# Performance work log

Measured on AMD Instinct MI355X. Metric: run time of the kernel, lower is better.

Reference implementation:

```python
import jax, jax.numpy as jnp
import numpy as np

N_NODES = 50000
N_EDGES = 1600000
N_FEAT = 128
DROPOUT = 0.1


def setup_inputs() -> dict:
    key = jax.random.key(0)
    k1, k2, k3, k4 = jax.random.split(key, 4)
    x = jax.random.normal(k1, (N_NODES, N_FEAT), dtype=jnp.float32)
    adj_vals = jax.random.uniform(k2, (N_EDGES,), dtype=jnp.float32)
    row = jax.random.randint(k3, (N_EDGES,), 0, N_NODES, dtype=jnp.int32)
    col = jax.random.randint(k4, (N_EDGES,), 0, N_NODES, dtype=jnp.int32)
    return {"x": x, "adj_vals": adj_vals, "row": row, "col": col}


def reference(x, adj_vals, row, col):
    # MixedDropout on sparse adjacency values (deterministic fixed key),
    # then SpMM: out[i] = sum_{e: row[e]==i} A_drop[e] * x[col[e]]
    keep_prob = 1.0 - DROPOUT
    mask_key = jax.random.fold_in(jax.random.key(42), 7)
    keep = jax.random.bernoulli(mask_key, keep_prob, adj_vals.shape)
    vals_drop = jnp.where(keep, adj_vals / keep_prob, 0.0)
    # gather source features and weight by (dropped) edge values
    msgs = vals_drop[:, None] * x[col]  # [E, F]
    out = jax.ops.segment_sum(msgs, row, num_segments=N_NODES)  # [N, F]
    return out
```

## Files before the change

### kernel.cpp

```cpp
#include <hip/hip_runtime.h>
#include <stdint.h>

#define N_NODES 50000
#define N_EDGES 1600000
#define N_FEAT 128
#define CAP 64
#define OVF_CAP 65536

#define NB 98
#define RSHIFT 9
#define NWG_A 256
#define CAPW 88
#define EPW (N_EDGES / NWG_A)


struct KeyPair { uint32_t a, b; };

__host__ __device__ constexpr inline uint32_t rotl32(uint32_t x, int r) {
  return (x << r) | (x >> (32 - r));
}

__host__ __device__ constexpr inline KeyPair threefry2x32(uint32_t k0, uint32_t k1,
                                                          uint32_t x0, uint32_t x1) {
  const uint32_t ks0 = k0, ks1 = k1, ks2 = k0 ^ k1 ^ 0x1BD11BDAu;
  x0 += ks0;
  x1 += ks1;
  const int rotA[4] = {13, 15, 26, 6};
  const int rotB[4] = {17, 29, 16, 24};
  const uint32_t ks[3] = {ks0, ks1, ks2};
  for (int i = 0; i < 5; ++i) {
    const int* rot = (i & 1) ? rotB : rotA;
    for (int j = 0; j < 4; ++j) {
      x0 += x1;
      x1 = rotl32(x1, rot[j]);
      x1 ^= x0;
    }
    x0 += ks[(i + 1) % 3];
    x1 += ks[(i + 2) % 3] + (uint32_t)(i + 1);
  }
  return {x0, x1};
}

constexpr KeyPair MASK_KEY = threefry2x32(0u, 42u, 0u, 7u);

__device__ inline bool edge_keep(uint32_t e) {
  KeyPair r = threefry2x32(MASK_KEY.a, MASK_KEY.b, 0u, e);
  uint32_t bits = r.a ^ r.b;
  float u = __uint_as_float((bits >> 9) | 0x3f800000u) - 1.0f;
  return u < 0.9f;
}

__device__ inline uint32_t f2bf(uint32_t b) {
  return (b + 0x7fffu + ((b >> 16) & 1u)) >> 16;
}


__global__ void __launch_bounds__(256) conv_bf16_kernel(const float* __restrict__ x,
                                                        uint32_t* __restrict__ xb) {
  int i = blockIdx.x * blockDim.x + threadIdx.x;
  if (i >= (N_NODES * N_FEAT) / 4) return;
  float4 f = ((const float4*)x)[i];
  uint2 o;
  o.x = f2bf(__float_as_uint(f.x)) | (f2bf(__float_as_uint(f.y)) << 16);
  o.y = f2bf(__float_as_uint(f.z)) | (f2bf(__float_as_uint(f.w)) << 16);
  ((uint2*)xb)[i] = o;
}

__global__ void __launch_bounds__(256) partA_kernel(const float* __restrict__ adj_vals,
                                                    const int* __restrict__ row,
                                                    const int* __restrict__ col,
                                                    uint64_t* __restrict__ coarse,
                                                    uint32_t* __restrict__ lens,
                                                    uint32_t* __restrict__ ovf_count,
                                                    uint64_t* __restrict__ ovf) {
  __shared__ uint32_t cnt[NB];
  int wg = blockIdx.x;
  int tid = threadIdx.x;
  if (tid < NB) cnt[tid] = 0;
  __syncthreads();
  int e0 = wg * EPW;
  int e1 = e0 + EPW;
  for (int e = e0 + tid; e < e1; e += 256) {
    if (!edge_keep((uint32_t)e)) continue;
    float v = adj_vals[e] / 0.9f;
    uint32_t r = (uint32_t)row[e];
    uint32_t c = (uint32_t)col[e];
    uint32_t b = r >> RSHIFT;
    uint32_t li = atomicAdd(&cnt[b], 1u);
    uint64_t p = ((uint64_t)r << 48) | ((uint64_t)c << 32) | (uint64_t)__float_as_uint(v);
    if (li < CAPW) {
      coarse[((size_t)b * NWG_A + wg) * CAPW + li] = p;
    } else {
      uint32_t oi = atomicAdd(ovf_count, 1u);
      if (oi < OVF_CAP) ovf[oi] = p;
    }
  }
  __syncthreads();
  if (tid < NB) lens[(size_t)tid * NWG_A + wg] = min(cnt[tid], (uint32_t)CAPW);
}

__global__ void __launch_bounds__(1024) partB_kernel(const uint64_t* __restrict__ coarse,
                                                     const uint32_t* __restrict__ lens,
                                                     uint64_t* __restrict__ payload,
                                                     uint32_t* __restrict__ cursor,
                                                     uint32_t* __restrict__ ovf_count,
                                                     uint64_t* __restrict__ ovf) {
  int b = blockIdx.x;
  int tid = threadIdx.x;
  __shared__ uint32_t s[NWG_A];
  __shared__ uint32_t cnt[512];
  if (tid < NWG_A) s[tid] = lens[(size_t)b * NWG_A + tid];
  if (tid < 512) cnt[tid] = 0;
  __syncthreads();
  for (int off = 1; off < NWG_A; off <<= 1) {
    uint32_t v = 0, u = 0;
    if (tid < NWG_A) {
      v = s[tid];
      u = (tid >= off) ? s[tid - off] : 0u;
    }
    __syncthreads();
    if (tid < NWG_A) s[tid] = v + u;
    __syncthreads();
  }
  uint32_t total = s[NWG_A - 1];
  for (uint32_t t = tid; t < total; t += 1024) {
    int lo = 0, hi = NWG_A - 1;
    while (lo < hi) {
      int mid = (lo + hi) >> 1;
      if (s[mid] > t) hi = mid; else lo = mid + 1;
    }
    uint32_t prev = lo ? s[lo - 1] : 0u;
    uint64_t p = coarse[((size_t)b * NWG_A + lo) * CAPW + (t - prev)];
    uint32_t r = (uint32_t)(p >> 48);
    uint32_t rl = r - ((uint32_t)b << RSHIFT);
    uint32_t idx = atomicAdd(&cnt[rl], 1u);
    if (idx < CAP) {
      payload[(size_t)r * CAP + idx] = p & 0x0000FFFFFFFFFFFFull;
    } else {
      uint32_t oi = atomicAdd(ovf_count, 1u);
      if (oi < OVF_CAP) ovf[oi] = p;
    }
  }
  __syncthreads();
  for (int k = tid; k < 512; k += 1024) {
    uint32_t r = ((uint32_t)b << RSHIFT) + (uint32_t)k;
    if (r < N_NODES) {
      uint32_t c0 = min(cnt[k], (uint32_t)CAP);
      cursor[r] = r * CAP + c0;
      uint32_t np = min((c0 + 7u) & ~7u, (uint32_t)CAP);
      for (uint32_t i2 = c0; i2 < np; ++i2) payload[(size_t)r * CAP + i2] = 0ull;
    }
  }
}

__global__ void __launch_bounds__(256) gather_bf16_kernel(const uint32_t* __restrict__ xb,
                                                          const uint64_t* __restrict__ payload,
                                                          const uint32_t* __restrict__ cursor,
                                                          float* __restrict__ out) {
  int r = blockIdx.x * 8 + (threadIdx.x >> 5);
  int lane = threadIdx.x & 31;
  uint32_t base = (uint32_t)r * CAP;
  uint32_t cnt = cursor[r] - base;
  uint32_t n = (cnt + 7u) & ~7u;
  const uint2* x2 = (const uint2*)xb;
  float4 acc = make_float4(0.f, 0.f, 0.f, 0.f);

  uint64_t p = payload[base + lane];
  int pc = (int)(p >> 32);
  float pv = __uint_as_float((uint32_t)p);

#define GSTEP(cc, vv)                                                        \
  {                                                                          \
    uint2 a = x2[(size_t)(cc) * 32 + lane];                                  \
    float f0 = __uint_as_float(a.x << 16);                                   \
    float f1 = __uint_as_float(a.x & 0xffff0000u);                           \
    float f2 = __uint_as_float(a.y << 16);                                   \
    float f3 = __uint_as_float(a.y & 0xffff0000u);                           \
    acc.x += (vv) * f0; acc.y += (vv) * f1;                                  \
    acc.z += (vv) * f2; acc.w += (vv) * f3;                                  \
  }

  int n0 = (int)min(n, 32u);
  for (int j = 0; j < n0; j += 8) {
    int   c0 = __shfl(pc, j + 0, 32); float v0 = __shfl(pv, j + 0, 32);
    int   c1 = __shfl(pc, j + 1, 32); float v1 = __shfl(pv, j + 1, 32);
    int   c2 = __shfl(pc, j + 2, 32); float v2 = __shfl(pv, j + 2, 32);
    int   c3 = __shfl(pc, j + 3, 32); float v3 = __shfl(pv, j + 3, 32);
    int   c4 = __shfl(pc, j + 4, 32); float v4 = __shfl(pv, j + 4, 32);
    int   c5 = __shfl(pc, j + 5, 32); float v5 = __shfl(pv, j + 5, 32);
    int   c6 = __shfl(pc, j + 6, 32); float v6 = __shfl(pv, j + 6, 32);
    int   c7 = __shfl(pc, j + 7, 32); float v7 = __shfl(pv, j + 7, 32);
    GSTEP(c0, v0) GSTEP(c1, v1) GSTEP(c2, v2) GSTEP(c3, v3)
    GSTEP(c4, v4) GSTEP(c5, v5) GSTEP(c6, v6) GSTEP(c7, v7)
  }
  if (n > 32) {
    uint64_t q = payload[base + 32 + lane];
    int qc = (int)(q >> 32);
    float qv = __uint_as_float((uint32_t)q);
    int n1 = (int)(n - 32u);
    for (int j = 0; j < n1; j += 8) {
      int   c0 = __shfl(qc, j + 0, 32); float v0 = __shfl(qv, j + 0, 32);
      int   c1 = __shfl(qc, j + 1, 32); float v1 = __shfl(qv, j + 1, 32);
      int   c2 = __shfl(qc, j + 2, 32); float v2 = __shfl(qv, j + 2, 32);
      int   c3 = __shfl(qc, j + 3, 32); float v3 = __shfl(qv, j + 3, 32);
      int   c4 = __shfl(qc, j + 4, 32); float v4 = __shfl(qv, j + 4, 32);
      int   c5 = __shfl(qc, j + 5, 32); float v5 = __shfl(qv, j + 5, 32);
      int   c6 = __shfl(qc, j + 6, 32); float v6 = __shfl(qv, j + 6, 32);
      int   c7 = __shfl(qc, j + 7, 32); float v7 = __shfl(qv, j + 7, 32);
      GSTEP(c0, v0) GSTEP(c1, v1) GSTEP(c2, v2) GSTEP(c3, v3)
      GSTEP(c4, v4) GSTEP(c5, v5) GSTEP(c6, v6) GSTEP(c7, v7)
    }
  }
#undef GSTEP
  ((float4*)out)[(size_t)r * 32 + lane] = acc;
}

__global__ void __launch_bounds__(256) ovf_pack_kernel(const float* __restrict__ x,
                                                       const uint32_t* __restrict__ ovf_count,
                                                       const uint64_t* __restrict__ ovf,
                                                       float* __restrict__ out) {
  uint32_t n = *ovf_count;
  if (n > OVF_CAP) n = OVF_CAP;
  int g = (int)((blockIdx.x * blockDim.x + threadIdx.x) >> 7);
  int f = threadIdx.x & 127;
  const int ngroups = (64 * 256) >> 7;
  for (uint32_t oi = g; oi < n; oi += ngroups) {
    uint64_t p = ovf[oi];
    uint32_t r = (uint32_t)(p >> 48);
    uint32_t c = (uint32_t)((p >> 32) & 0xFFFFu);
    float v = __uint_as_float((uint32_t)p);
    atomicAdd(&out[(size_t)r * N_FEAT + f], v * x[(size_t)c * N_FEAT + f]);
  }
}


__global__ void __launch_bounds__(128) gather_shfl_kernel(const float* __restrict__ x,
                                                          const uint64_t* __restrict__ payload,
                                                          const uint32_t* __restrict__ cursor,
                                                          float* __restrict__ out) {
  int r = blockIdx.x * 4 + (threadIdx.x >> 5);
  int lane = threadIdx.x & 31;
  uint32_t base = (uint32_t)r * CAP;
  uint32_t cnt = cursor[r] - base;
  uint32_t n = (cnt + 7u) & ~7u;
  const float4* x4 = (const float4*)x;
  float4 acc = make_float4(0.f, 0.f, 0.f, 0.f);
  uint64_t p = payload[base + lane];
  int pc = (int)(p >> 32);
  float pv = __uint_as_float((uint32_t)p);
  int n0 = (int)min(n, 32u);
  for (int j = 0; j < n0; j += 8) {
    int   c0 = __shfl(pc, j + 0, 32); float v0 = __shfl(pv, j + 0, 32);
    int   c1 = __shfl(pc, j + 1, 32); float v1 = __shfl(pv, j + 1, 32);
    int   c2 = __shfl(pc, j + 2, 32); float v2 = __shfl(pv, j + 2, 32);
    int   c3 = __shfl(pc, j + 3, 32); float v3 = __shfl(pv, j + 3, 32);
    int   c4 = __shfl(pc, j + 4, 32); float v4 = __shfl(pv, j + 4, 32);
    int   c5 = __shfl(pc, j + 5, 32); float v5 = __shfl(pv, j + 5, 32);
    int   c6 = __shfl(pc, j + 6, 32); float v6 = __shfl(pv, j + 6, 32);
    int   c7 = __shfl(pc, j + 7, 32); float v7 = __shfl(pv, j + 7, 32);
    float4 a0 = x4[(size_t)c0 * 32 + lane];
    float4 a1 = x4[(size_t)c1 * 32 + lane];
    float4 a2 = x4[(size_t)c2 * 32 + lane];
    float4 a3 = x4[(size_t)c3 * 32 + lane];
    float4 a4 = x4[(size_t)c4 * 32 + lane];
    float4 a5 = x4[(size_t)c5 * 32 + lane];
    float4 a6 = x4[(size_t)c6 * 32 + lane];
    float4 a7 = x4[(size_t)c7 * 32 + lane];
    acc.x += v0 * a0.x; acc.y += v0 * a0.y; acc.z += v0 * a0.z; acc.w += v0 * a0.w;
    acc.x += v1 * a1.x; acc.y += v1 * a1.y; acc.z += v1 * a1.z; acc.w += v1 * a1.w;
    acc.x += v2 * a2.x; acc.y += v2 * a2.y; acc.z += v2 * a2.z; acc.w += v2 * a2.w;
    acc.x += v3 * a3.x; acc.y += v3 * a3.y; acc.z += v3 * a3.z; acc.w += v3 * a3.w;
    acc.x += v4 * a4.x; acc.y += v4 * a4.y; acc.z += v4 * a4.z; acc.w += v4 * a4.w;
    acc.x += v5 * a5.x; acc.y += v5 * a5.y; acc.z += v5 * a5.z; acc.w += v5 * a5.w;
    acc.x += v6 * a6.x; acc.y += v6 * a6.y; acc.z += v6 * a6.z; acc.w += v6 * a6.w;
    acc.x += v7 * a7.x; acc.y += v7 * a7.y; acc.z += v7 * a7.z; acc.w += v7 * a7.w;
  }
  if (n > 32) {
    uint64_t q = payload[base + 32 + lane];
    int qc = (int)(q >> 32);
    float qv = __uint_as_float((uint32_t)q);
    int n1 = (int)(n - 32u);
    for (int j = 0; j < n1; j += 8) {
      int   c0 = __shfl(qc, j + 0, 32); float v0 = __shfl(qv, j + 0, 32);
      int   c1 = __shfl(qc, j + 1, 32); float v1 = __shfl(qv, j + 1, 32);
      int   c2 = __shfl(qc, j + 2, 32); float v2 = __shfl(qv, j + 2, 32);
      int   c3 = __shfl(qc, j + 3, 32); float v3 = __shfl(qv, j + 3, 32);
      int   c4 = __shfl(qc, j + 4, 32); float v4 = __shfl(qv, j + 4, 32);
      int   c5 = __shfl(qc, j + 5, 32); float v5 = __shfl(qv, j + 5, 32);
      int   c6 = __shfl(qc, j + 6, 32); float v6 = __shfl(qv, j + 6, 32);
      int   c7 = __shfl(qc, j + 7, 32); float v7 = __shfl(qv, j + 7, 32);
      float4 a0 = x4[(size_t)c0 * 32 + lane];
      float4 a1 = x4[(size_t)c1 * 32 + lane];
      float4 a2 = x4[(size_t)c2 * 32 + lane];
      float4 a3 = x4[(size_t)c3 * 32 + lane];
      float4 a4 = x4[(size_t)c4 * 32 + lane];
      float4 a5 = x4[(size_t)c5 * 32 + lane];
      float4 a6 = x4[(size_t)c6 * 32 + lane];
      float4 a7 = x4[(size_t)c7 * 32 + lane];
      acc.x += v0 * a0.x; acc.y += v0 * a0.y; acc.z += v0 * a0.z; acc.w += v0 * a0.w;
      acc.x += v1 * a1.x; acc.y += v1 * a1.y; acc.z += v1 * a1.z; acc.w += v1 * a1.w;
      acc.x += v2 * a2.x; acc.y += v2 * a2.y; acc.z += v2 * a2.z; acc.w += v2 * a2.w;
      acc.x += v3 * a3.x; acc.y += v3 * a3.y; acc.z += v3 * a3.z; acc.w += v3 * a3.w;
      acc.x += v4 * a4.x; acc.y += v4 * a4.y; acc.z += v4 * a4.z; acc.w += v4 * a4.w;
      acc.x += v5 * a5.x; acc.y += v5 * a5.y; acc.z += v5 * a5.z; acc.w += v5 * a5.w;
      acc.x += v6 * a6.x; acc.y += v6 * a6.y; acc.z += v6 * a6.z; acc.w += v6 * a6.w;
      acc.x += v7 * a7.x; acc.y += v7 * a7.y; acc.z += v7 * a7.z; acc.w += v7 * a7.w;
    }
  }
  ((float4*)out)[(size_t)r * 32 + lane] = acc;
}


__global__ void __launch_bounds__(256) scatter_fused_kernel(const float* __restrict__ x,
                                                            const float* __restrict__ adj_vals,
                                                            const int* __restrict__ row,
                                                            const int* __restrict__ col,
                                                            float* __restrict__ out) {
  long long t = (long long)blockIdx.x * blockDim.x + threadIdx.x;
  int e = (int)(t >> 6);
  int lane = (int)(t & 63);
  if (e >= N_EDGES) return;
  if (!edge_keep((uint32_t)e)) return;
  float v = adj_vals[e] / 0.9f;
  float2 xf = *(const float2*)(x + (long long)col[e] * N_FEAT + lane * 2);
  float* dst = out + (long long)row[e] * N_FEAT + lane * 2;
  atomicAdd(dst, v * xf.x);
  atomicAdd(dst + 1, v * xf.y);
}


extern "C" void kernel_launch(void* const* d_in, const int* in_sizes, int n_in,
                              void* d_out, int out_size, void* d_ws, size_t ws_size,
                              hipStream_t stream) {
  const float* x        = (const float*)d_in[0];
  const float* adj_vals = (const float*)d_in[1];
  const int*   row      = (const int*)d_in[2];
  const int*   col      = (const int*)d_in[3];
  float* out = (float*)d_out;

  size_t a_cursor  = 0;
  size_t a_ovfc    = (a_cursor + (size_t)N_NODES * 4 + 255) & ~255ull;
  size_t a_ovf     = (a_ovfc + 4 + 255) & ~255ull;
  size_t a_lens    = (a_ovf + (size_t)OVF_CAP * 8 + 255) & ~255ull;
  size_t a_coarse  = (a_lens + (size_t)NB * NWG_A * 4 + 255) & ~255ull;
  size_t a_payload = (a_coarse + (size_t)NB * NWG_A * CAPW * 8 + 255) & ~255ull;
  size_t radix_need = a_payload + (size_t)N_NODES * CAP * 8;
  size_t a_xb      = (radix_need + 255) & ~255ull;
  size_t radix_bf16_need = a_xb + (size_t)N_NODES * N_FEAT * 2;

  if (ws_size >= radix_need) {
    uint32_t* cursor    = (uint32_t*)((char*)d_ws + a_cursor);
    uint32_t* ovf_count = (uint32_t*)((char*)d_ws + a_ovfc);
    uint64_t* ovf       = (uint64_t*)((char*)d_ws + a_ovf);
    uint32_t* lens      = (uint32_t*)((char*)d_ws + a_lens);
    uint64_t* coarse    = (uint64_t*)((char*)d_ws + a_coarse);
    uint64_t* payload   = (uint64_t*)((char*)d_ws + a_payload);

    hipMemsetAsync(ovf_count, 0, 4, stream);
    bool use_bf16 = (ws_size >= radix_bf16_need);
    if (use_bf16) {
      uint32_t* xb = (uint32_t*)((char*)d_ws + a_xb);
      conv_bf16_kernel<<<(N_NODES * N_FEAT / 4 + 255) / 256, 256, 0, stream>>>(x, xb);
      partA_kernel<<<NWG_A, 256, 0, stream>>>(adj_vals, row, col, coarse, lens, ovf_count, ovf);
      partB_kernel<<<NB, 1024, 0, stream>>>(coarse, lens, payload, cursor, ovf_count, ovf);
      gather_bf16_kernel<<<N_NODES / 8, 256, 0, stream>>>(xb, payload, cursor, out);
    } else {
      partA_kernel<<<NWG_A, 256, 0, stream>>>(adj_vals, row, col, coarse, lens, ovf_count, ovf);
      partB_kernel<<<NB, 1024, 0, stream>>>(coarse, lens, payload, cursor, ovf_count, ovf);
      gather_shfl_kernel<<<N_NODES / 4, 128, 0, stream>>>(x, payload, cursor, out);
    }
    ovf_pack_kernel<<<64, 256, 0, stream>>>(x, ovf_count, ovf, out);
  } else {
    hipMemsetAsync(d_out, 0, (size_t)out_size * sizeof(float), stream);
    long long total_threads = (long long)N_EDGES * 64;
    scatter_fused_kernel<<<(int)((total_threads + 255) / 256), 256, 0, stream>>>(
        x, adj_vals, row, col, out);
  }
}
```

Before: 178.9 us.

## Fuse bf16 conversion into partition pass, pack payload to 32-bit, finer buckets

Merges the x-to-bf16 conversion kernel into the first partition kernel, which now runs with 1024 threads per block, removing one launch. Shrinks bucket granularity to 256 rows (196 buckets) and replaces partB's per-element binary search with a fixed 4-threads-per-segment walk. Packs each payload entry into 32 bits (16-bit column plus bf16 value), halving payload traffic and the shuffles in gather. The 16-bit column only covers node indices below 65536 and rounding edge values to bf16 adds error. The fp32 fallback gather path is removed.

```diff
diff --git a/kernel.cpp b/kernel.cpp
--- a/kernel.cpp
+++ b/kernel.cpp
@@ -7,10 +7,12 @@
 #define CAP 64
 #define OVF_CAP 65536
 
-#define NB 98
-#define RSHIFT 9
+#define RSHIFT 8
+#define BROWS 256
+#define NB 196
 #define NWG_A 256
-#define CAPW 88
+#define A_THREADS 1024
+#define CAPW 56
 #define EPW (N_EDGES / NWG_A)
 
 
@@ -55,32 +57,33 @@
 }
 
 
-__global__ void __launch_bounds__(256) conv_bf16_kernel(const float* __restrict__ x,
-                                                        uint32_t* __restrict__ xb) {
-  int i = blockIdx.x * blockDim.x + threadIdx.x;
-  if (i >= (N_NODES * N_FEAT) / 4) return;
-  float4 f = ((const float4*)x)[i];
-  uint2 o;
-  o.x = f2bf(__float_as_uint(f.x)) | (f2bf(__float_as_uint(f.y)) << 16);
-  o.y = f2bf(__float_as_uint(f.z)) | (f2bf(__float_as_uint(f.w)) << 16);
-  ((uint2*)xb)[i] = o;
-}
-
-__global__ void __launch_bounds__(256) partA_kernel(const float* __restrict__ adj_vals,
-                                                    const int* __restrict__ row,
-                                                    const int* __restrict__ col,
-                                                    uint64_t* __restrict__ coarse,
-                                                    uint32_t* __restrict__ lens,
-                                                    uint32_t* __restrict__ ovf_count,
-                                                    uint64_t* __restrict__ ovf) {
+__global__ void __launch_bounds__(A_THREADS) convA_kernel(const float* __restrict__ x,
+                                                          uint32_t* __restrict__ xb,
+                                                          const float* __restrict__ adj_vals,
+                                                          const int* __restrict__ row,
+                                                          const int* __restrict__ col,
+                                                          uint64_t* __restrict__ coarse,
+                                                          uint32_t* __restrict__ lens,
+                                                          uint32_t* __restrict__ ovf_count,
+                                                          uint64_t* __restrict__ ovf) {
   __shared__ uint32_t cnt[NB];
   int wg = blockIdx.x;
   int tid = threadIdx.x;
   if (tid < NB) cnt[tid] = 0;
-  __syncthreads();
+
+  const int gthreads = NWG_A * A_THREADS;
+  for (int i = wg * A_THREADS + tid; i < (N_NODES * N_FEAT) / 4; i += gthreads) {
+    float4 f = ((const float4*)x)[i];
+    uint2 o;
+    o.x = f2bf(__float_as_uint(f.x)) | (f2bf(__float_as_uint(f.y)) << 16);
+    o.y = f2bf(__float_as_uint(f.z)) | (f2bf(__float_as_uint(f.w)) << 16);
+    ((uint2*)xb)[i] = o;
+  }
+  __syncthreads();
+
   int e0 = wg * EPW;
   int e1 = e0 + EPW;
-  for (int e = e0 + tid; e < e1; e += 256) {
+  for (int e = e0 + tid; e < e1; e += A_THREADS) {
     if (!edge_keep((uint32_t)e)) continue;
     float v = adj_vals[e] / 0.9f;
     uint32_t r = (uint32_t)row[e];
@@ -101,16 +104,16 @@
 
 __global__ void __launch_bounds__(1024) partB_kernel(const uint64_t* __restrict__ coarse,
                                                      const uint32_t* __restrict__ lens,
-                                                     uint64_t* __restrict__ payload,
+                                                     uint32_t* __restrict__ payload,
                                                      uint32_t* __restrict__ cursor,
                                                      uint32_t* __restrict__ ovf_count,
                                                      uint64_t* __restrict__ ovf) {
   int b = blockIdx.x;
   int tid = threadIdx.x;
   __shared__ uint32_t s[NWG_A];
-  __shared__ uint32_t cnt[512];
+  __shared__ uint32_t cnt[BROWS];
   if (tid < NWG_A) s[tid] = lens[(size_t)b * NWG_A + tid];
-  if (tid < 512) cnt[tid] = 0;
+  if (tid < BROWS) cnt[tid] = 0;
   __syncthreads();
   for (int off = 1; off < NWG_A; off <<= 1) {
     uint32_t v = 0, u = 0;
@@ -122,39 +125,38 @@
     if (tid < NWG_A) s[tid] = v + u;
     __syncthreads();
   }
-  uint32_t total = s[NWG_A - 1];
-  for (uint32_t t = tid; t < total; t += 1024) {
-    int lo = 0, hi = NWG_A - 1;
-    while (lo < hi) {
-      int mid = (lo + hi) >> 1;
-      if (s[mid] > t) hi = mid; else lo = mid + 1;
-    }
-    uint32_t prev = lo ? s[lo - 1] : 0u;
-    uint64_t p = coarse[((size_t)b * NWG_A + lo) * CAPW + (t - prev)];
+  int seg = tid >> 2;
+  int sub = tid & 3;
+  uint32_t sbase = (seg == 0) ? 0u : s[seg - 1];
+  uint32_t slen = s[seg] - sbase;
+  const uint64_t* cseg = coarse + ((size_t)b * NWG_A + seg) * CAPW;
+  for (uint32_t li = (uint32_t)sub; li < slen; li += 4) {
+    uint64_t p = cseg[li];
     uint32_t r = (uint32_t)(p >> 48);
-    uint32_t rl = r - ((uint32_t)b << RSHIFT);
+    uint32_t rl = r & (BROWS - 1);
     uint32_t idx = atomicAdd(&cnt[rl], 1u);
     if (idx < CAP) {
-      payload[(size_t)r * CAP + idx] = p & 0x0000FFFFFFFFFFFFull;
+      uint32_t c = (uint32_t)(p >> 32) & 0xFFFFu;
+      payload[(size_t)r * CAP + idx] = (c << 16) | f2bf((uint32_t)p);
     } else {
       uint32_t oi = atomicAdd(ovf_count, 1u);
       if (oi < OVF_CAP) ovf[oi] = p;
     }
   }
   __syncthreads();
-  for (int k = tid; k < 512; k += 1024) {
+  for (int k = tid; k < BROWS; k += 1024) {
     uint32_t r = ((uint32_t)b << RSHIFT) + (uint32_t)k;
     if (r < N_NODES) {
       uint32_t c0 = min(cnt[k], (uint32_t)CAP);
       cursor[r] = r * CAP + c0;
       uint32_t np = min((c0 + 7u) & ~7u, (uint32_t)CAP);
-      for (uint32_t i2 = c0; i2 < np; ++i2) payload[(size_t)r * CAP + i2] = 0ull;
+      for (uint32_t i2 = c0; i2 < np; ++i2) payload[(size_t)r * CAP + i2] = 0u;
     }
   }
 }
 
 __global__ void __launch_bounds__(256) gather_bf16_kernel(const uint32_t* __restrict__ xb,
-                                                          const uint64_t* __restrict__ payload,
+                                                          const uint32_t* __restrict__ payload,
                                                           const uint32_t* __restrict__ cursor,
                                                           float* __restrict__ out) {
   int r = blockIdx.x * 8 + (threadIdx.x >> 5);
@@ -165,50 +167,48 @@
   const uint2* x2 = (const uint2*)xb;
   float4 acc = make_float4(0.f, 0.f, 0.f, 0.f);
 
-  uint64_t p = payload[base + lane];
-  int pc = (int)(p >> 32);
-  float pv = __uint_as_float((uint32_t)p);
-
-#define GSTEP(cc, vv)                                                        \
+  uint32_t p = payload[base + lane];
+
+#define GSTEP(ww)                                                            \
   {                                                                          \
-    uint2 a = x2[(size_t)(cc) * 32 + lane];                                  \
+    uint32_t cc = (ww) >> 16;                                                \
+    float vv = __uint_as_float((ww) << 16);                                  \
+    uint2 a = x2[(size_t)cc * 32 + lane];                                    \
     float f0 = __uint_as_float(a.x << 16);                                   \
     float f1 = __uint_as_float(a.x & 0xffff0000u);                           \
     float f2 = __uint_as_float(a.y << 16);                                   \
     float f3 = __uint_as_float(a.y & 0xffff0000u);                           \
-    acc.x += (vv) * f0; acc.y += (vv) * f1;                                  \
-    acc.z += (vv) * f2; acc.w += (vv) * f3;                                  \
+    acc.x += vv * f0; acc.y += vv * f1;                                      \
+    acc.z += vv * f2; acc.w += vv * f3;                                      \
   }
 
   int n0 = (int)min(n, 32u);
   for (int j = 0; j < n0; j += 8) {
-    int   c0 = __shfl(pc, j + 0, 32); float v0 = __shfl(pv, j + 0, 32);
-    int   c1 = __shfl(pc, j + 1, 32); float v1 = __shfl(pv, j + 1, 32);
-    int   c2 = __shfl(pc, j + 2, 32); float v2 = __shfl(pv, j + 2, 32);
-    int   c3 = __shfl(pc, j + 3, 32); float v3 = __shfl(pv, j + 3, 32);
-    int   c4 = __shfl(pc, j + 4, 32); float v4 = __shfl(pv, j + 4, 32);
-    int   c5 = __shfl(pc, j + 5, 32); float v5 = __shfl(pv, j + 5, 32);
-    int   c6 = __shfl(pc, j + 6, 32); float v6 = __shfl(pv, j + 6, 32);
-    int   c7 = __shfl(pc, j + 7, 32); float v7 = __shfl(pv, j + 7, 32);
-    GSTEP(c0, v0) GSTEP(c1, v1) GSTEP(c2, v2) GSTEP(c3, v3)
-    GSTEP(c4, v4) GSTEP(c5, v5) GSTEP(c6, v6) GSTEP(c7, v7)
+    uint32_t w0 = __shfl(p, j + 0, 32);
+    uint32_t w1 = __shfl(p, j + 1, 32);
+    uint32_t w2 = __shfl(p, j + 2, 32);
+    uint32_t w3 = __shfl(p, j + 3, 32);
+    uint32_t w4 = __shfl(p, j + 4, 32);
+    uint32_t w5 = __shfl(p, j + 5, 32);
+    uint32_t w6 = __shfl(p, j + 6, 32);
+    uint32_t w7 = __shfl(p, j + 7, 32);
+    GSTEP(w0) GSTEP(w1) GSTEP(w2) GSTEP(w3)
+    GSTEP(w4) GSTEP(w5) GSTEP(w6) GSTEP(w7)
   }
   if (n > 32) {
-    uint64_t q = payload[base + 32 + lane];
-    int qc = (int)(q >> 32);
-    float qv = __uint_as_float((uint32_t)q);
+    uint32_t q = payload[base + 32 + lane];
     int n1 = (int)(n - 32u);
     for (int j = 0; j < n1; j += 8) {
-      int   c0 = __shfl(qc, j + 0, 32); float v0 = __shfl(qv, j + 0, 32);
-      int   c1 = __shfl(qc, j + 1, 32); float v1 = __shfl(qv, j + 1, 32);
-      int   c2 = __shfl(qc, j + 2, 32); float v2 = __shfl(qv, j + 2, 32);
-      int   c3 = __shfl(qc, j + 3, 32); float v3 = __shfl(qv, j + 3, 32);
-      int   c4 = __shfl(qc, j + 4, 32); float v4 = __shfl(qv, j + 4, 32);
-      int   c5 = __shfl(qc, j + 5, 32); float v5 = __shfl(qv, j + 5, 32);
-      int   c6 = __shfl(qc, j + 6, 32); float v6 = __shfl(qv, j + 6, 32);
-      int   c7 = __shfl(qc, j + 7, 32); float v7 = __shfl(qv, j + 7, 32);
-      GSTEP(c0, v0) GSTEP(c1, v1) GSTEP(c2, v2) GSTEP(c3, v3)
-      GSTEP(c4, v4) GSTEP(c5, v5) GSTEP(c6, v6) GSTEP(c7, v7)
+      uint32_t w0 = __shfl(q, j + 0, 32);
+      uint32_t w1 = __shfl(q, j + 1, 32);
+      uint32_t w2 = __shfl(q, j + 2, 32);
+      uint32_t w3 = __shfl(q, j + 3, 32);
+      uint32_t w4 = __shfl(q, j + 4, 32);
+      uint32_t w5 = __shfl(q, j + 5, 32);
+      uint32_t w6 = __shfl(q, j + 6, 32);
+      uint32_t w7 = __shfl(q, j + 7, 32);
+      GSTEP(w0) GSTEP(w1) GSTEP(w2) GSTEP(w3)
+      GSTEP(w4) GSTEP(w5) GSTEP(w6) GSTEP(w7)
     }
   }
 #undef GSTEP
@@ -234,83 +234,6 @@
 }
 
 
-__global__ void __launch_bounds__(128) gather_shfl_kernel(const float* __restrict__ x,
-                                                          const uint64_t* __restrict__ payload,
-                                                          const uint32_t* __restrict__ cursor,
-                                                          float* __restrict__ out) {
-  int r = blockIdx.x * 4 + (threadIdx.x >> 5);
-  int lane = threadIdx.x & 31;
-  uint32_t base = (uint32_t)r * CAP;
-  uint32_t cnt = cursor[r] - base;
-  uint32_t n = (cnt + 7u) & ~7u;
-  const float4* x4 = (const float4*)x;
-  float4 acc = make_float4(0.f, 0.f, 0.f, 0.f);
-  uint64_t p = payload[base + lane];
-  int pc = (int)(p >> 32);
-  float pv = __uint_as_float((uint32_t)p);
-  int n0 = (int)min(n, 32u);
-  for (int j = 0; j < n0; j += 8) {
-    int   c0 = __shfl(pc, j + 0, 32); float v0 = __shfl(pv, j + 0, 32);
-    int   c1 = __shfl(pc, j + 1, 32); float v1 = __shfl(pv, j + 1, 32);
-    int   c2 = __shfl(pc, j + 2, 32); float v2 = __shfl(pv, j + 2, 32);
-    int   c3 = __shfl(pc, j + 3, 32); float v3 = __shfl(pv, j + 3, 32);
-    int   c4 = __shfl(pc, j + 4, 32); float v4 = __shfl(pv, j + 4, 32);
-    int   c5 = __shfl(pc, j + 5, 32); float v5 = __shfl(pv, j + 5, 32);
-    int   c6 = __shfl(pc, j + 6, 32); float v6 = __shfl(pv, j + 6, 32);
-    int   c7 = __shfl(pc, j + 7, 32); float v7 = __shfl(pv, j + 7, 32);
-    float4 a0 = x4[(size_t)c0 * 32 + lane];
-    float4 a1 = x4[(size_t)c1 * 32 + lane];
-    float4 a2 = x4[(size_t)c2 * 32 + lane];
-    float4 a3 = x4[(size_t)c3 * 32 + lane];
-    float4 a4 = x4[(size_t)c4 * 32 + lane];
-    float4 a5 = x4[(size_t)c5 * 32 + lane];
-    float4 a6 = x4[(size_t)c6 * 32 + lane];
-    float4 a7 = x4[(size_t)c7 * 32 + lane];
-    acc.x += v0 * a0.x; acc.y += v0 * a0.y; acc.z += v0 * a0.z; acc.w += v0 * a0.w;
-    acc.x += v1 * a1.x; acc.y += v1 * a1.y; acc.z += v1 * a1.z; acc.w += v1 * a1.w;
-    acc.x += v2 * a2.x; acc.y += v2 * a2.y; acc.z += v2 * a2.z; acc.w += v2 * a2.w;
-    acc.x += v3 * a3.x; acc.y += v3 * a3.y; acc.z += v3 * a3.z; acc.w += v3 * a3.w;
-    acc.x += v4 * a4.x; acc.y += v4 * a4.y; acc.z += v4 * a4.z; acc.w += v4 * a4.w;
-    acc.x += v5 * a5.x; acc.y += v5 * a5.y; acc.z += v5 * a5.z; acc.w += v5 * a5.w;
-    acc.x += v6 * a6.x; acc.y += v6 * a6.y; acc.z += v6 * a6.z; acc.w += v6 * a6.w;
-    acc.x += v7 * a7.x; acc.y += v7 * a7.y; acc.z += v7 * a7.z; acc.w += v7 * a7.w;
-  }
-  if (n > 32) {
-    uint64_t q = payload[base + 32 + lane];
-    int qc = (int)(q >> 32);
-    float qv = __uint_as_float((uint32_t)q);
-    int n1 = (int)(n - 32u);
-    for (int j = 0; j < n1; j += 8) {
-      int   c0 = __shfl(qc, j + 0, 32); float v0 = __shfl(qv, j + 0, 32);
-      int   c1 = __shfl(qc, j + 1, 32); float v1 = __shfl(qv, j + 1, 32);
-      int   c2 = __shfl(qc, j + 2, 32); float v2 = __shfl(qv, j + 2, 32);
-      int   c3 = __shfl(qc, j + 3, 32); float v3 = __shfl(qv, j + 3, 32);
-      int   c4 = __shfl(qc, j + 4, 32); float v4 = __shfl(qv, j + 4, 32);
-      int   c5 = __shfl(qc, j + 5, 32); float v5 = __shfl(qv, j + 5, 32);
-      int   c6 = __shfl(qc, j + 6, 32); float v6 = __shfl(qv, j + 6, 32);
-      int   c7 = __shfl(qc, j + 7, 32); float v7 = __shfl(qv, j + 7, 32);
-      float4 a0 = x4[(size_t)c0 * 32 + lane];
-      float4 a1 = x4[(size_t)c1 * 32 + lane];
-      float4 a2 = x4[(size_t)c2 * 32 + lane];
-      float4 a3 = x4[(size_t)c3 * 32 + lane];
-      float4 a4 = x4[(size_t)c4 * 32 + lane];
-      float4 a5 = x4[(size_t)c5 * 32 + lane];
-      float4 a6 = x4[(size_t)c6 * 32 + lane];
-      float4 a7 = x4[(size_t)c7 * 32 + lane];
-      acc.x += v0 * a0.x; acc.y += v0 * a0.y; acc.z += v0 * a0.z; acc.w += v0 * a0.w;
-      acc.x += v1 * a1.x; acc.y += v1 * a1.y; acc.z += v1 * a1.z; acc.w += v1 * a1.w;
-      acc.x += v2 * a2.x; acc.y += v2 * a2.y; acc.z += v2 * a2.z; acc.w += v2 * a2.w;
-      acc.x += v3 * a3.x; acc.y += v3 * a3.y; acc.z += v3 * a3.z; acc.w += v3 * a3.w;
-      acc.x += v4 * a4.x; acc.y += v4 * a4.y; acc.z += v4 * a4.z; acc.w += v4 * a4.w;
-      acc.x += v5 * a5.x; acc.y += v5 * a5.y; acc.z += v5 * a5.z; acc.w += v5 * a5.w;
-      acc.x += v6 * a6.x; acc.y += v6 * a6.y; acc.z += v6 * a6.z; acc.w += v6 * a6.w;
-      acc.x += v7 * a7.x; acc.y += v7 * a7.y; acc.z += v7 * a7.z; acc.w += v7 * a7.w;
-    }
-  }
-  ((float4*)out)[(size_t)r * 32 + lane] = acc;
-}
-
-
 __global__ void __launch_bounds__(256) scatter_fused_kernel(const float* __restrict__ x,
                                                             const float* __restrict__ adj_vals,
                                                             const int* __restrict__ row,
@@ -344,31 +267,23 @@
   size_t a_lens    = (a_ovf + (size_t)OVF_CAP * 8 + 255) & ~255ull;
   size_t a_coarse  = (a_lens + (size_t)NB * NWG_A * 4 + 255) & ~255ull;
   size_t a_payload = (a_coarse + (size_t)NB * NWG_A * CAPW * 8 + 255) & ~255ull;
-  size_t radix_need = a_payload + (size_t)N_NODES * CAP * 8;
-  size_t a_xb      = (radix_need + 255) & ~255ull;
-  size_t radix_bf16_need = a_xb + (size_t)N_NODES * N_FEAT * 2;
-
-  if (ws_size >= radix_need) {
+  size_t a_xb      = (a_payload + (size_t)N_NODES * CAP * 4 + 255) & ~255ull;
+  size_t need      = a_xb + (size_t)N_NODES * N_FEAT * 2;
+
+  if (ws_size >= need) {
     uint32_t* cursor    = (uint32_t*)((char*)d_ws + a_cursor);
     uint32_t* ovf_count = (uint32_t*)((char*)d_ws + a_ovfc);
     uint64_t* ovf       = (uint64_t*)((char*)d_ws + a_ovf);
     uint32_t* lens      = (uint32_t*)((char*)d_ws + a_lens);
     uint64_t* coarse    = (uint64_t*)((char*)d_ws + a_coarse);
-    uint64_t* payload   = (uint64_t*)((char*)d_ws + a_payload);
+    uint32_t* payload   = (uint32_t*)((char*)d_ws + a_payload);
+    uint32_t* xb        = (uint32_t*)((char*)d_ws + a_xb);
 
     hipMemsetAsync(ovf_count, 0, 4, stream);
-    bool use_bf16 = (ws_size >= radix_bf16_need);
-    if (use_bf16) {
-      uint32_t* xb = (uint32_t*)((char*)d_ws + a_xb);
-      conv_bf16_kernel<<<(N_NODES * N_FEAT / 4 + 255) / 256, 256, 0, stream>>>(x, xb);
-      partA_kernel<<<NWG_A, 256, 0, stream>>>(adj_vals, row, col, coarse, lens, ovf_count, ovf);
-      partB_kernel<<<NB, 1024, 0, stream>>>(coarse, lens, payload, cursor, ovf_count, ovf);
-      gather_bf16_kernel<<<N_NODES / 8, 256, 0, stream>>>(xb, payload, cursor, out);
-    } else {
-      partA_kernel<<<NWG_A, 256, 0, stream>>>(adj_vals, row, col, coarse, lens, ovf_count, ovf);
-      partB_kernel<<<NB, 1024, 0, stream>>>(coarse, lens, payload, cursor, ovf_count, ovf);
-      gather_shfl_kernel<<<N_NODES / 4, 128, 0, stream>>>(x, payload, cursor, out);
-    }
+    convA_kernel<<<NWG_A, A_THREADS, 0, stream>>>(x, xb, adj_vals, row, col,
+                                                  coarse, lens, ovf_count, ovf);
+    partB_kernel<<<NB, 1024, 0, stream>>>(coarse, lens, payload, cursor, ovf_count, ovf);
+    gather_bf16_kernel<<<N_NODES / 8, 256, 0, stream>>>(xb, payload, cursor, out);
     ovf_pack_kernel<<<64, 256, 0, stream>>>(x, ovf_count, ovf, out);
   } else {
     hipMemsetAsync(d_out, 0, (size_t)out_size * sizeof(float), stream);
```

Result: faster. 169.1 us (-5.5%).
